# Performance work log

Hardware: AMD Instinct MI355X
Metric: run time of the kernel (lower is better)

## Reference

```python
import jax, jax.numpy as jnp
import numpy as np

PEAK_THRESH = 0.2
PEAK_WEIGHT = 5.0
FOCAL_GAMMA = 2.0
ALPHA_COUNT, ALPHA_HEATMAP, ALPHA_CONF = 1.0, 10.0, 1.5
EPS = 1e-6


def setup_inputs() -> dict:
    key = jax.random.key(0)
    k1, k2, k3, k4, k5, k6 = jax.random.split(key, 6)
    B, P, K, H, W = 16, 20, 17, 64, 64
    return {
        "count_logits": jax.random.normal(k1, (B, P + 1), dtype=jnp.float32),
        "pred_heatmaps": jax.random.normal(k2, (B, P, K, H, W), dtype=jnp.float32),
        "pred_conf_logits": jax.random.normal(k3, (B, P), dtype=jnp.float32),
        "gt_heatmaps": jax.random.uniform(k4, (B, P, K, H, W), dtype=jnp.float32),
        "count": jax.random.randint(k5, (B,), 0, P + 1, dtype=jnp.int32),
        "mask": jax.random.randint(k6, (B, P), 0, 2, dtype=jnp.int32),
    }


def _cross_entropy(logits, labels):
    logp = jax.nn.log_softmax(logits, axis=-1)
    return -jnp.mean(jnp.take_along_axis(logp, labels[:, None], axis=-1))


def _peak_mse(pred, gt, mask_f):
    # weight map: 1 everywhere, PEAK_WEIGHT where gt > thresh
    w = jnp.where(gt > PEAK_THRESH, PEAK_WEIGHT, 1.0)
    m = mask_f[:, :, None, None, None]  # [B,P,1,1,1]
    diff = (pred - gt) ** 2 * w * m
    B, P, K, H, W = pred.shape
    return diff.sum() / (mask_f.sum() * K * H * W + EPS)


def _focal_loss(logits, targets):
    # stable BCE-with-logits, elementwise
    bce = jnp.maximum(logits, 0.0) - logits * targets + jnp.log1p(jnp.exp(-jnp.abs(logits)))
    p_t = jnp.exp(-bce)
    return jnp.mean((1.0 - p_t) ** FOCAL_GAMMA * bce)


def reference(count_logits, pred_heatmaps, pred_conf_logits, gt_heatmaps, count, mask):
    mask_f = mask.astype(pred_heatmaps.dtype)
    loss_count = _cross_entropy(count_logits, count)
    hm = _peak_mse(pred_heatmaps, gt_heatmaps, mask_f)
    loss_heatmap = jnp.where(mask_f.sum() > 0, hm, 0.0)
    loss_conf = _focal_loss(pred_conf_logits, mask_f)
    total = ALPHA_COUNT * loss_count + ALPHA_HEATMAP * loss_heatmap + ALPHA_CONF * loss_conf
    return total
```

## Files before the change

kernel.cpp:

```cpp
#include <hip/hip_runtime.h>
#include <hip/hip_bf16.h>


#define B_      16
#define P_      20
#define NBP     (B_ * P_)
#define KHW     (17 * 64 * 64)
#define KHW4    (KHW / 4)
#define TOTAL4  (NBP * KHW4)
#define NBLOCKS 4096
#define NTHREADS 256

#define PEAK_THRESH 0.2f
#define PEAK_WEIGHT 5.0f

__global__ __launch_bounds__(NTHREADS)
void hm_partial_kernel(const float4* __restrict__ pred,
                       const float4* __restrict__ gt,
                       const int*    __restrict__ mask,
                       float*        __restrict__ partial) {
    float acc = 0.0f;
    const int stride = gridDim.x * blockDim.x;
    for (int i = blockIdx.x * blockDim.x + threadIdx.x; i < TOTAL4; i += stride) {
        const int slice = i / KHW4;
        if (mask[slice] != 0) {
            const float4 p = pred[i];
            const float4 g = gt[i];
            float d, w;
            d = p.x - g.x; w = (g.x > PEAK_THRESH) ? PEAK_WEIGHT : 1.0f; acc += d * d * w;
            d = p.y - g.y; w = (g.y > PEAK_THRESH) ? PEAK_WEIGHT : 1.0f; acc += d * d * w;
            d = p.z - g.z; w = (g.z > PEAK_THRESH) ? PEAK_WEIGHT : 1.0f; acc += d * d * w;
            d = p.w - g.w; w = (g.w > PEAK_THRESH) ? PEAK_WEIGHT : 1.0f; acc += d * d * w;
        }
    }
    #pragma unroll
    for (int off = 32; off > 0; off >>= 1) acc += __shfl_down(acc, off);

    __shared__ float s[NTHREADS / 64];
    if ((threadIdx.x & 63) == 0) s[threadIdx.x >> 6] = acc;
    __syncthreads();
    if (threadIdx.x == 0) {
        float t = 0.0f;
        #pragma unroll
        for (int w = 0; w < NTHREADS / 64; ++w) t += s[w];
        partial[blockIdx.x] = t;
    }
}

__global__ __launch_bounds__(64)
void finalize_kernel(const float* __restrict__ partial,
                     const float* __restrict__ count_logits,
                     const int*   __restrict__ count,
                     const float* __restrict__ conf_logits,
                     const int*   __restrict__ mask,
                     float*       __restrict__ out) {
    const int lane = threadIdx.x;

    float ds = 0.0f;
    for (int i = lane; i < NBLOCKS; i += 64) ds += partial[i];

    float ms = 0.0f, fs = 0.0f;
    for (int i = lane; i < NBP; i += 64) {
        const float t = (float)mask[i];
        ms += t;
        const float l   = conf_logits[i];
        const float bce = fmaxf(l, 0.0f) - l * t + log1pf(expf(-fabsf(l)));
        const float pt  = expf(-bce);
        const float om  = 1.0f - pt;
        fs += om * om * bce;
    }

    float ce = 0.0f;
    if (lane < B_) {
        const float* row = count_logits + lane * (P_ + 1);
        float mx = row[0];
        #pragma unroll
        for (int j = 1; j < P_ + 1; ++j) mx = fmaxf(mx, row[j]);
        float se = 0.0f;
        #pragma unroll
        for (int j = 0; j < P_ + 1; ++j) se += expf(row[j] - mx);
        const float lse = mx + logf(se);
        ce = -(row[count[lane]] - lse);
    }

    #pragma unroll
    for (int off = 32; off > 0; off >>= 1) {
        ds += __shfl_down(ds, off);
        ms += __shfl_down(ms, off);
        fs += __shfl_down(fs, off);
        ce += __shfl_down(ce, off);
    }

    if (lane == 0) {
        const float loss_count = ce / (float)B_;
        const float loss_conf  = fs / (float)NBP;
        const float hm         = ds / (ms * (float)KHW + 1e-6f);
        const float loss_hm    = (ms > 0.0f) ? hm : 0.0f;
        out[0] = 1.0f * loss_count + 10.0f * loss_hm + 1.5f * loss_conf;
    }
}

extern "C" void kernel_launch(void* const* d_in, const int* in_sizes, int n_in,
                              void* d_out, int out_size, void* d_ws, size_t ws_size,
                              hipStream_t stream) {
    const float* count_logits = (const float*)d_in[0];
    const float* pred_hm      = (const float*)d_in[1];
    const float* conf_logits  = (const float*)d_in[2];
    const float* gt_hm        = (const float*)d_in[3];
    const int*   count        = (const int*)d_in[4];
    const int*   mask         = (const int*)d_in[5];
    float*       out          = (float*)d_out;
    float*       partial      = (float*)d_ws;

    hm_partial_kernel<<<NBLOCKS, NTHREADS, 0, stream>>>(
        (const float4*)pred_hm, (const float4*)gt_hm, mask, partial);

    finalize_kernel<<<1, 64, 0, stream>>>(
        partial, count_logits, count, conf_logits, mask, out);
}
```

Measured before the change: 203.3 us.

## Map blocks to per-slice chunks with early exit on masked slices

Replaces the grid-stride loop with a 2D grid where each block handles one 1024-float4 chunk of a single (batch, person) slice, issuing eight independent float4 loads per thread. Blocks for masked-out slices write zero and return immediately, removing per-iteration division and mask checks. This raises memory-level parallelism and balances load, at the cost of more blocks and more partial sums to reduce in finalize.

```diff
diff --git a/kernel.cpp b/kernel.cpp
--- a/kernel.cpp
+++ b/kernel.cpp
@@ -7,43 +7,55 @@
 #define NBP     (B_ * P_)
 #define KHW     (17 * 64 * 64)
 #define KHW4    (KHW / 4)
-#define TOTAL4  (NBP * KHW4)
-#define NBLOCKS 4096
+#define CHUNKS  17
+#define NPART   (NBP * CHUNKS)
 #define NTHREADS 256
 
 #define PEAK_THRESH 0.2f
 #define PEAK_WEIGHT 5.0f
+
+__device__ __forceinline__ float wdiff4(float4 p, float4 g) {
+    float d, w, a = 0.0f;
+    d = p.x - g.x; w = (g.x > PEAK_THRESH) ? PEAK_WEIGHT : 1.0f; a = fmaf(d * d, w, a);
+    d = p.y - g.y; w = (g.y > PEAK_THRESH) ? PEAK_WEIGHT : 1.0f; a = fmaf(d * d, w, a);
+    d = p.z - g.z; w = (g.z > PEAK_THRESH) ? PEAK_WEIGHT : 1.0f; a = fmaf(d * d, w, a);
+    d = p.w - g.w; w = (g.w > PEAK_THRESH) ? PEAK_WEIGHT : 1.0f; a = fmaf(d * d, w, a);
+    return a;
+}
 
 __global__ __launch_bounds__(NTHREADS)
 void hm_partial_kernel(const float4* __restrict__ pred,
                        const float4* __restrict__ gt,
                        const int*    __restrict__ mask,
                        float*        __restrict__ partial) {
-    float acc = 0.0f;
-    const int stride = gridDim.x * blockDim.x;
-    for (int i = blockIdx.x * blockDim.x + threadIdx.x; i < TOTAL4; i += stride) {
-        const int slice = i / KHW4;
-        if (mask[slice] != 0) {
-            const float4 p = pred[i];
-            const float4 g = gt[i];
-            float d, w;
-            d = p.x - g.x; w = (g.x > PEAK_THRESH) ? PEAK_WEIGHT : 1.0f; acc += d * d * w;
-            d = p.y - g.y; w = (g.y > PEAK_THRESH) ? PEAK_WEIGHT : 1.0f; acc += d * d * w;
-            d = p.z - g.z; w = (g.z > PEAK_THRESH) ? PEAK_WEIGHT : 1.0f; acc += d * d * w;
-            d = p.w - g.w; w = (g.w > PEAK_THRESH) ? PEAK_WEIGHT : 1.0f; acc += d * d * w;
-        }
+    const int s    = blockIdx.y;
+    const int pidx = s * CHUNKS + blockIdx.x;
+    if (mask[s] == 0) {
+        if (threadIdx.x == 0) partial[pidx] = 0.0f;
+        return;
     }
+    const int base = s * KHW4 + blockIdx.x * (NTHREADS * 4) + threadIdx.x;
+
+    const float4 p0 = pred[base];
+    const float4 p1 = pred[base + 256];
+    const float4 p2 = pred[base + 512];
+    const float4 p3 = pred[base + 768];
+    const float4 g0 = gt[base];
+    const float4 g1 = gt[base + 256];
+    const float4 g2 = gt[base + 512];
+    const float4 g3 = gt[base + 768];
+
+    float acc = (wdiff4(p0, g0) + wdiff4(p1, g1)) + (wdiff4(p2, g2) + wdiff4(p3, g3));
+
     #pragma unroll
     for (int off = 32; off > 0; off >>= 1) acc += __shfl_down(acc, off);
 
-    __shared__ float s[NTHREADS / 64];
-    if ((threadIdx.x & 63) == 0) s[threadIdx.x >> 6] = acc;
+    __shared__ float sm[NTHREADS / 64];
+    if ((threadIdx.x & 63) == 0) sm[threadIdx.x >> 6] = acc;
     __syncthreads();
     if (threadIdx.x == 0) {
-        float t = 0.0f;
-        #pragma unroll
-        for (int w = 0; w < NTHREADS / 64; ++w) t += s[w];
-        partial[blockIdx.x] = t;
+        float t = (sm[0] + sm[1]) + (sm[2] + sm[3]);
+        partial[pidx] = t;
     }
 }
 
@@ -57,7 +69,7 @@
     const int lane = threadIdx.x;
 
     float ds = 0.0f;
-    for (int i = lane; i < NBLOCKS; i += 64) ds += partial[i];
+    for (int i = lane; i < NPART; i += 64) ds += partial[i];
 
     float ms = 0.0f, fs = 0.0f;
     for (int i = lane; i < NBP; i += 64) {
@@ -112,7 +124,8 @@
     float*       out          = (float*)d_out;
     float*       partial      = (float*)d_ws;
 
-    hm_partial_kernel<<<NBLOCKS, NTHREADS, 0, stream>>>(
+    dim3 grid(CHUNKS, NBP);
+    hm_partial_kernel<<<grid, NTHREADS, 0, stream>>>(
         (const float4*)pred_hm, (const float4*)gt_hm, mask, partial);
 
     finalize_kernel<<<1, 64, 0, stream>>>(
```

New measurement: 207.3 us. No clear change (+1.9%).
